# Kernel tuning notes

Measured on AMD Instinct MI355X. Metric: run time of the kernel, lower is better.

Reference implementation:

```python
import jax, jax.numpy as jnp
import numpy as np


def setup_inputs() -> dict:
    key = jax.random.key(0)
    k0, k1, k2 = jax.random.split(key, 3)
    B, C, N, M = 2, 64, 1024, 32
    C_mid = 16  # bottleneck of the AFA weight-learning MLP (C -> C//4 -> C)
    feature = jax.random.normal(k0, (B, C, N, M), dtype=jnp.float32)
    W1 = (jax.random.normal(k1, (C_mid, C), dtype=jnp.float32) / np.float32(np.sqrt(C)))
    b1 = jnp.zeros((C_mid,), dtype=jnp.float32)
    W2 = (jax.random.normal(k2, (C, C_mid), dtype=jnp.float32) / np.float32(np.sqrt(C_mid)))
    b2 = jnp.zeros((C,), dtype=jnp.float32)
    return {"feature": feature, "W1": W1, "b1": b1, "W2": W2, "b2": b2}


def reference(feature, W1, b1, W2, b2):
    # feature: (B, C, N, M)
    B, C, N, M = feature.shape
    eye = jnp.eye(M, dtype=feature.dtype)  # (M, M)
    # pair[b,c,n,i,j] = f_i - f_j + f_i * delta_ij  (the repeat/transpose/eye trick)
    fi = feature[..., :, None]                      # (B, C, N, M, 1)
    pair = fi - feature[..., None, :] + fi * eye    # (B, C, N, M, M)
    # 1x1-conv MLP over channel dim (SharedMLP: C -> C_mid -> C), ReLU between
    h = jax.nn.relu(jnp.einsum('oc,bcnij->bonij', W1, pair)
                    + b1[None, :, None, None, None])
    w = (jnp.einsum('oc,bcnij->bonij', W2, h)
         + b2[None, :, None, None, None])           # (B, C, N, M, M)
    w = jax.nn.softmax(w, axis=-1)                  # use_softmax=True, over last dim
    # weighted-sum aggregation over j -> (B, C, N, M)
    return jnp.sum(pair * w, axis=-1)
```

## Files before the change

### kernel.cpp

```cpp
#include <hip/hip_runtime.h>
#include <stdint.h>

namespace {
constexpr int NM = 1024 * 32;
constexpr float LOG2E = 1.44269504088896340736f;

typedef _Float16 half8 __attribute__((ext_vector_type(8)));
typedef float floatx16 __attribute__((ext_vector_type(16)));
typedef float f2v __attribute__((ext_vector_type(2)));

__device__ __forceinline__ uint32_t pkrtz_bits(float a, float b) {
  auto pk = __builtin_amdgcn_cvt_pkrtz(a, b);
  uint32_t u;
  __builtin_memcpy(&u, &pk, 4);
  return u;
}

__global__ __launch_bounds__(256, 4) void afa_kernel(
    const float* __restrict__ feat,
    const float* __restrict__ W1,
    const float* __restrict__ b1,
    const float* __restrict__ W2,
    float* __restrict__ out)
{
  __shared__ __align__(16) float f_c[64 * 34];
  __shared__ __align__(16) float g1b[32 * 20];
  __shared__ __align__(16) float edia[64 * 34];
  __shared__ __align__(16) float outs[64 * 34];

  const int t = threadIdx.x;
  const int bn = blockIdx.x;
  const size_t base = (size_t)(bn >> 10) * (64 * NM) + (size_t)(bn & 1023) * 32;

  const int w  = t >> 6;
  const int ln = t & 63;
  const int cl = ln & 31;
  const int hl = ln >> 5;

  half8 B0, B1;
  {
    const float4* w2a = reinterpret_cast<const float4*>(W2 + cl * 16 + 8 * hl);
    const float4 x = w2a[0], y = w2a[1];
    B0[0] = (_Float16)(x.x * LOG2E); B0[1] = (_Float16)(x.y * LOG2E);
    B0[2] = (_Float16)(x.z * LOG2E); B0[3] = (_Float16)(x.w * LOG2E);
    B0[4] = (_Float16)(y.x * LOG2E); B0[5] = (_Float16)(y.y * LOG2E);
    B0[6] = (_Float16)(y.z * LOG2E); B0[7] = (_Float16)(y.w * LOG2E);
    const float4* w2b = reinterpret_cast<const float4*>(W2 + (cl + 32) * 16 + 8 * hl);
    const float4 u = w2b[0], v = w2b[1];
    B1[0] = (_Float16)(u.x * LOG2E); B1[1] = (_Float16)(u.y * LOG2E);
    B1[2] = (_Float16)(u.z * LOG2E); B1[3] = (_Float16)(u.w * LOG2E);
    B1[4] = (_Float16)(v.x * LOG2E); B1[5] = (_Float16)(v.y * LOG2E);
    B1[6] = (_Float16)(v.z * LOG2E); B1[7] = (_Float16)(v.w * LOG2E);
  }

  {
    const int m = t & 31, c0 = t >> 5;
    #pragma unroll
    for (int r = 0; r < 8; ++r) {
      const int c = c0 + 8 * r;
      f_c[c * 34 + m] = feat[base + (size_t)c * NM + m];
    }
  }
  __syncthreads();

  floatx16 Z;
  #pragma unroll
  for (int r = 0; r < 16; ++r) Z[r] = 0.f;

  if (w == 0) {
    floatx16 Cg = Z;
    #pragma unroll
    for (int ch = 0; ch < 4; ++ch) {
      union { half8 h; uint32_t u[4]; } Af;
      if (cl < 16) {
        const float4 a0 = *reinterpret_cast<const float4*>(W1 + cl * 64 + 16 * ch + 8 * hl);
        const float4 a1 = *reinterpret_cast<const float4*>(W1 + cl * 64 + 16 * ch + 8 * hl + 4);
        Af.u[0] = pkrtz_bits(a0.x, a0.y);
        Af.u[1] = pkrtz_bits(a0.z, a0.w);
        Af.u[2] = pkrtz_bits(a1.x, a1.y);
        Af.u[3] = pkrtz_bits(a1.z, a1.w);
      } else {
        Af.u[0] = 0; Af.u[1] = 0; Af.u[2] = 0; Af.u[3] = 0;
      }
      union { half8 h; uint32_t u[4]; } Bf;
      #pragma unroll
      for (int p = 0; p < 4; ++p) {
        const int c = 16 * ch + 8 * hl + 2 * p;
        Bf.u[p] = pkrtz_bits(f_c[c * 34 + cl], f_c[(c + 1) * 34 + cl]);
      }
      Cg = __builtin_amdgcn_mfma_f32_32x32x16_f16(Af.h, Bf.h, Cg, 0, 0, 0);
    }
    const float4 bb0 = *reinterpret_cast<const float4*>(b1 + 4 * hl);
    const float4 bb1 = *reinterpret_cast<const float4*>(b1 + 8 + 4 * hl);
    const float4 g0 = {Cg[0] + bb0.x, Cg[1] + bb0.y, Cg[2] + bb0.z, Cg[3] + bb0.w};
    const float4 g1v = {Cg[4] + bb1.x, Cg[5] + bb1.y, Cg[6] + bb1.z, Cg[7] + bb1.w};
    *reinterpret_cast<float4*>(g1b + cl * 20 + 4 * hl) = g0;
    *reinterpret_cast<float4*>(g1b + cl * 20 + 8 + 4 * hl) = g1v;

    const uint32_t pk0 = pkrtz_bits(fmaxf(g0.x, 0.f), fmaxf(g0.y, 0.f));
    const uint32_t pk1 = pkrtz_bits(fmaxf(g0.z, 0.f), fmaxf(g0.w, 0.f));
    const uint32_t pk2 = pkrtz_bits(fmaxf(g1v.x, 0.f), fmaxf(g1v.y, 0.f));
    const uint32_t pk3 = pkrtz_bits(fmaxf(g1v.z, 0.f), fmaxf(g1v.w, 0.f));
    const uint32_t px0 = (uint32_t)__shfl_xor((int)pk0, 32);
    const uint32_t px1 = (uint32_t)__shfl_xor((int)pk1, 32);
    const uint32_t px2 = (uint32_t)__shfl_xor((int)pk2, 32);
    const uint32_t px3 = (uint32_t)__shfl_xor((int)pk3, 32);
    union { half8 h; uint32_t u[4]; } au;
    if (hl == 0) { au.u[0] = pk0; au.u[1] = pk1; au.u[2] = px0; au.u[3] = px1; }
    else         { au.u[0] = px2; au.u[1] = px3; au.u[2] = pk2; au.u[3] = pk3; }
    floatx16 d0 = __builtin_amdgcn_mfma_f32_32x32x16_f16(au.h, B0, Z, 0, 0, 0);
    floatx16 d1 = __builtin_amdgcn_mfma_f32_32x32x16_f16(au.h, B1, Z, 0, 0, 0);
    #pragma unroll
    for (int r = 0; r < 16; ++r) {
      const int ir = (r & 3) + 8 * (r >> 2) + 4 * hl;
      edia[cl * 34 + ir]        = __builtin_amdgcn_exp2f(d0[r]);
      edia[(cl + 32) * 34 + ir] = __builtin_amdgcn_exp2f(d1[r]);
    }
  }

  float fcol0[16], fcol1[16];
  #pragma unroll
  for (int q = 0; q < 4; ++q) {
    const int jr = 8 * q + 4 * hl;
    const float2 a0 = *reinterpret_cast<const float2*>(f_c + cl * 34 + jr);
    const float2 a1 = *reinterpret_cast<const float2*>(f_c + cl * 34 + jr + 2);
    fcol0[4 * q]     = a0.x; fcol0[4 * q + 1] = a0.y;
    fcol0[4 * q + 2] = a1.x; fcol0[4 * q + 3] = a1.y;
    const float2 c0v = *reinterpret_cast<const float2*>(f_c + (cl + 32) * 34 + jr);
    const float2 c1v = *reinterpret_cast<const float2*>(f_c + (cl + 32) * 34 + jr + 2);
    fcol1[4 * q]     = c0v.x; fcol1[4 * q + 1] = c0v.y;
    fcol1[4 * q + 2] = c1v.x; fcol1[4 * q + 3] = c1v.y;
  }
  __syncthreads();

  float gjn[8];
  {
    const float4* gp = reinterpret_cast<const float4*>(g1b + cl * 20 + 8 * hl);
    const float4 x = gp[0], y = gp[1];
    const float4* bb = reinterpret_cast<const float4*>(b1 + 8 * hl);
    const float4 bx = bb[0], by = bb[1];
    gjn[0] = bx.x - x.x; gjn[1] = bx.y - x.y; gjn[2] = bx.z - x.z; gjn[3] = bx.w - x.w;
    gjn[4] = by.x - y.x; gjn[5] = by.y - y.y; gjn[6] = by.z - y.z; gjn[7] = by.w - y.w;
  }

  #pragma unroll 1
  for (int ii = 0; ii < 8; ++ii) {
    const int i = w * 8 + ii;
    const bool dg = (cl == i);
    const float4* gi4 = reinterpret_cast<const float4*>(g1b + i * 20 + 8 * hl);
    const float4 gx = gi4[0], gy = gi4[1];
    const float gi[8] = {gx.x, gx.y, gx.z, gx.w, gy.x, gy.y, gy.z, gy.w};
    union { half8 h; uint32_t u[4]; } au;
    #pragma unroll
    for (int p = 0; p < 4; ++p) {
      const float h0 = fmaxf(gi[2 * p]     + (dg ? 0.f : gjn[2 * p]),     0.f);
      const float h1 = fmaxf(gi[2 * p + 1] + (dg ? 0.f : gjn[2 * p + 1]), 0.f);
      au.u[p] = pkrtz_bits(h0, h1);
    }
    const floatx16 acc0 = __builtin_amdgcn_mfma_f32_32x32x16_f16(au.h, B0, Z, 0, 0, 0);
    const floatx16 acc1 = __builtin_amdgcn_mfma_f32_32x32x16_f16(au.h, B1, Z, 0, 0, 0);

    f2v S0 = {0.f, 0.f}, D0 = {0.f, 0.f}, S1 = {0.f, 0.f}, D1 = {0.f, 0.f};
    #pragma unroll
    for (int r = 0; r < 16; r += 2) {
      const f2v e0 = {__builtin_amdgcn_exp2f(acc0[r]),
                      __builtin_amdgcn_exp2f(acc0[r + 1])};
      const f2v fc0 = {fcol0[r], fcol0[r + 1]};
      S0 += e0;
      D0 += fc0 * e0;
      const f2v e1 = {__builtin_amdgcn_exp2f(acc1[r]),
                      __builtin_amdgcn_exp2f(acc1[r + 1])};
      const f2v fc1 = {fcol1[r], fcol1[r + 1]};
      S1 += e1;
      D1 += fc1 * e1;
    }
    float Sa = S0.x + S0.y, Da = D0.x + D0.y;
    float Sb = S1.x + S1.y, Db = D1.x + D1.y;
    Sa += __shfl_xor(Sa, 32); Da += __shfl_xor(Da, 32);
    Sb += __shfl_xor(Sb, 32); Db += __shfl_xor(Db, 32);

    const float fi0 = f_c[cl * 34 + i];
    const float fi1 = f_c[(cl + 32) * 34 + i];
    const float ei0 = edia[cl * 34 + i];
    const float ei1 = edia[(cl + 32) * 34 + i];
    const float inv0 = 1.0f / Sa;
    const float inv1 = 1.0f / Sb;
    outs[cl * 34 + i]        = fi0 * (1.0f + ei0 * inv0) - Da * inv0;
    outs[(cl + 32) * 34 + i] = fi1 * (1.0f + ei1 * inv1) - Db * inv1;
  }
  __syncthreads();

  {
    const int m = t & 31, c0 = t >> 5;
    #pragma unroll
    for (int r = 0; r < 8; ++r) {
      const int cc = c0 + 8 * r;
      out[base + (size_t)cc * NM + m] = outs[cc * 34 + m];
    }
  }
}
}

extern "C" void kernel_launch(void* const* d_in, const int* in_sizes, int n_in,
                              void* d_out, int out_size, void* d_ws, size_t ws_size,
                              hipStream_t stream) {
  const float* feat = (const float*)d_in[0];
  const float* W1   = (const float*)d_in[1];
  const float* b1   = (const float*)d_in[2];
  const float* W2   = (const float*)d_in[3];
  float* out = (float*)d_out;

  afa_kernel<<<dim3(2 * 1024), dim3(256), 0, stream>>>(feat, W1, b1, W2, out);
}
```

Before: 31.21 us.

## Process both batches per block and prefetch second batch during first compute

Each block now handles one n index for both batch elements, which halves the grid. The second batch's features are loaded into registers before the first compute, so that global latency is hidden behind it. W2 fragment setup is also amortized over two tiles. In exchange, register pressure rises and there are fewer blocks for occupancy and tail balance.

```diff
diff --git a/kernel.cpp b/kernel.cpp
--- a/kernel.cpp
+++ b/kernel.cpp
@@ -29,13 +29,16 @@
   __shared__ __align__(16) float outs[64 * 34];
 
   const int t = threadIdx.x;
-  const int bn = blockIdx.x;
-  const size_t base = (size_t)(bn >> 10) * (64 * NM) + (size_t)(bn & 1023) * 32;
+  const int n = blockIdx.x;
+  const size_t base0 = (size_t)n * 32;
+  const size_t base1 = (size_t)64 * NM + (size_t)n * 32;
 
   const int w  = t >> 6;
   const int ln = t & 63;
   const int cl = ln & 31;
   const int hl = ln >> 5;
+  const int m  = t & 31;
+  const int c0 = t >> 5;
 
   half8 B0, B1;
   {
@@ -52,151 +55,167 @@
     B1[4] = (_Float16)(v.x * LOG2E); B1[5] = (_Float16)(v.y * LOG2E);
     B1[6] = (_Float16)(v.z * LOG2E); B1[7] = (_Float16)(v.w * LOG2E);
   }
-
-  {
-    const int m = t & 31, c0 = t >> 5;
+  floatx16 Z;
+  #pragma unroll
+  for (int r = 0; r < 16; ++r) Z[r] = 0.f;
+
+  #pragma unroll
+  for (int r = 0; r < 8; ++r) {
+    const int c = c0 + 8 * r;
+    f_c[c * 34 + m] = feat[base0 + (size_t)c * NM + m];
+  }
+  __syncthreads();
+
+  float p1s[8];
+  #pragma unroll
+  for (int r = 0; r < 8; ++r) {
+    const int c = c0 + 8 * r;
+    p1s[r] = feat[base1 + (size_t)c * NM + m];
+  }
+
+  auto compute = [&]() {
+    if (w == 0) {
+      floatx16 Cg = Z;
+      #pragma unroll
+      for (int ch = 0; ch < 4; ++ch) {
+        union { half8 h; uint32_t u[4]; } Af;
+        if (cl < 16) {
+          const float4 a0 = *reinterpret_cast<const float4*>(W1 + cl * 64 + 16 * ch + 8 * hl);
+          const float4 a1 = *reinterpret_cast<const float4*>(W1 + cl * 64 + 16 * ch + 8 * hl + 4);
+          Af.u[0] = pkrtz_bits(a0.x, a0.y);
+          Af.u[1] = pkrtz_bits(a0.z, a0.w);
+          Af.u[2] = pkrtz_bits(a1.x, a1.y);
+          Af.u[3] = pkrtz_bits(a1.z, a1.w);
+        } else {
+          Af.u[0] = 0; Af.u[1] = 0; Af.u[2] = 0; Af.u[3] = 0;
+        }
+        union { half8 h; uint32_t u[4]; } Bf;
+        #pragma unroll
+        for (int p = 0; p < 4; ++p) {
+          const int c = 16 * ch + 8 * hl + 2 * p;
+          Bf.u[p] = pkrtz_bits(f_c[c * 34 + cl], f_c[(c + 1) * 34 + cl]);
+        }
+        Cg = __builtin_amdgcn_mfma_f32_32x32x16_f16(Af.h, Bf.h, Cg, 0, 0, 0);
+      }
+      const float4 bb0 = *reinterpret_cast<const float4*>(b1 + 4 * hl);
+      const float4 bb1 = *reinterpret_cast<const float4*>(b1 + 8 + 4 * hl);
+      const float4 g0 = {Cg[0] + bb0.x, Cg[1] + bb0.y, Cg[2] + bb0.z, Cg[3] + bb0.w};
+      const float4 g1v = {Cg[4] + bb1.x, Cg[5] + bb1.y, Cg[6] + bb1.z, Cg[7] + bb1.w};
+      *reinterpret_cast<float4*>(g1b + cl * 20 + 4 * hl) = g0;
+      *reinterpret_cast<float4*>(g1b + cl * 20 + 8 + 4 * hl) = g1v;
+
+      const uint32_t pk0 = pkrtz_bits(fmaxf(g0.x, 0.f), fmaxf(g0.y, 0.f));
+      const uint32_t pk1 = pkrtz_bits(fmaxf(g0.z, 0.f), fmaxf(g0.w, 0.f));
+      const uint32_t pk2 = pkrtz_bits(fmaxf(g1v.x, 0.f), fmaxf(g1v.y, 0.f));
+      const uint32_t pk3 = pkrtz_bits(fmaxf(g1v.z, 0.f), fmaxf(g1v.w, 0.f));
+      const uint32_t px0 = (uint32_t)__shfl_xor((int)pk0, 32);
+      const uint32_t px1 = (uint32_t)__shfl_xor((int)pk1, 32);
+      const uint32_t px2 = (uint32_t)__shfl_xor((int)pk2, 32);
+      const uint32_t px3 = (uint32_t)__shfl_xor((int)pk3, 32);
+      union { half8 h; uint32_t u[4]; } au;
+      if (hl == 0) { au.u[0] = pk0; au.u[1] = pk1; au.u[2] = px0; au.u[3] = px1; }
+      else         { au.u[0] = px2; au.u[1] = px3; au.u[2] = pk2; au.u[3] = pk3; }
+      floatx16 d0 = __builtin_amdgcn_mfma_f32_32x32x16_f16(au.h, B0, Z, 0, 0, 0);
+      floatx16 d1 = __builtin_amdgcn_mfma_f32_32x32x16_f16(au.h, B1, Z, 0, 0, 0);
+      #pragma unroll
+      for (int r = 0; r < 16; ++r) {
+        const int ir = (r & 3) + 8 * (r >> 2) + 4 * hl;
+        edia[cl * 34 + ir]        = __builtin_amdgcn_exp2f(d0[r]);
+        edia[(cl + 32) * 34 + ir] = __builtin_amdgcn_exp2f(d1[r]);
+      }
+    }
+
+    float fcol0[16], fcol1[16];
     #pragma unroll
-    for (int r = 0; r < 8; ++r) {
-      const int c = c0 + 8 * r;
-      f_c[c * 34 + m] = feat[base + (size_t)c * NM + m];
-    }
+    for (int q = 0; q < 4; ++q) {
+      const int jr = 8 * q + 4 * hl;
+      const float2 a0 = *reinterpret_cast<const float2*>(f_c + cl * 34 + jr);
+      const float2 a1 = *reinterpret_cast<const float2*>(f_c + cl * 34 + jr + 2);
+      fcol0[4 * q]     = a0.x; fcol0[4 * q + 1] = a0.y;
+      fcol0[4 * q + 2] = a1.x; fcol0[4 * q + 3] = a1.y;
+      const float2 c0v = *reinterpret_cast<const float2*>(f_c + (cl + 32) * 34 + jr);
+      const float2 c1v = *reinterpret_cast<const float2*>(f_c + (cl + 32) * 34 + jr + 2);
+      fcol1[4 * q]     = c0v.x; fcol1[4 * q + 1] = c0v.y;
+      fcol1[4 * q + 2] = c1v.x; fcol1[4 * q + 3] = c1v.y;
+    }
+    __syncthreads();
+
+    float gjn[8];
+    {
+      const float4* gp = reinterpret_cast<const float4*>(g1b + cl * 20 + 8 * hl);
+      const float4 x = gp[0], y = gp[1];
+      const float4* bb = reinterpret_cast<const float4*>(b1 + 8 * hl);
+      const float4 bx = bb[0], by = bb[1];
+      gjn[0] = bx.x - x.x; gjn[1] = bx.y - x.y; gjn[2] = bx.z - x.z; gjn[3] = bx.w - x.w;
+      gjn[4] = by.x - y.x; gjn[5] = by.y - y.y; gjn[6] = by.z - y.z; gjn[7] = by.w - y.w;
+    }
+
+    #pragma unroll 1
+    for (int ii = 0; ii < 8; ++ii) {
+      const int i = w * 8 + ii;
+      const bool dg = (cl == i);
+      const float4* gi4 = reinterpret_cast<const float4*>(g1b + i * 20 + 8 * hl);
+      const float4 gx = gi4[0], gy = gi4[1];
+      const float gi[8] = {gx.x, gx.y, gx.z, gx.w, gy.x, gy.y, gy.z, gy.w};
+      union { half8 h; uint32_t u[4]; } au;
+      #pragma unroll
+      for (int p = 0; p < 4; ++p) {
+        const float h0 = fmaxf(gi[2 * p]     + (dg ? 0.f : gjn[2 * p]),     0.f);
+        const float h1 = fmaxf(gi[2 * p + 1] + (dg ? 0.f : gjn[2 * p + 1]), 0.f);
+        au.u[p] = pkrtz_bits(h0, h1);
+      }
+      const floatx16 acc0 = __builtin_amdgcn_mfma_f32_32x32x16_f16(au.h, B0, Z, 0, 0, 0);
+      const floatx16 acc1 = __builtin_amdgcn_mfma_f32_32x32x16_f16(au.h, B1, Z, 0, 0, 0);
+
+      f2v S0 = {0.f, 0.f}, D0 = {0.f, 0.f}, S1 = {0.f, 0.f}, D1 = {0.f, 0.f};
+      #pragma unroll
+      for (int r = 0; r < 16; r += 2) {
+        const f2v e0 = {__builtin_amdgcn_exp2f(acc0[r]),
+                        __builtin_amdgcn_exp2f(acc0[r + 1])};
+        const f2v fc0 = {fcol0[r], fcol0[r + 1]};
+        S0 += e0;
+        D0 += fc0 * e0;
+        const f2v e1 = {__builtin_amdgcn_exp2f(acc1[r]),
+                        __builtin_amdgcn_exp2f(acc1[r + 1])};
+        const f2v fc1 = {fcol1[r], fcol1[r + 1]};
+        S1 += e1;
+        D1 += fc1 * e1;
+      }
+      float Sa = S0.x + S0.y, Da = D0.x + D0.y;
+      float Sb = S1.x + S1.y, Db = D1.x + D1.y;
+      Sa += __shfl_xor(Sa, 32); Da += __shfl_xor(Da, 32);
+      Sb += __shfl_xor(Sb, 32); Db += __shfl_xor(Db, 32);
+
+      const float fi0 = f_c[cl * 34 + i];
+      const float fi1 = f_c[(cl + 32) * 34 + i];
+      const float ei0 = edia[cl * 34 + i];
+      const float ei1 = edia[(cl + 32) * 34 + i];
+      const float inv0 = 1.0f / Sa;
+      const float inv1 = 1.0f / Sb;
+      outs[cl * 34 + i]        = fi0 * (1.0f + ei0 * inv0) - Da * inv0;
+      outs[(cl + 32) * 34 + i] = fi1 * (1.0f + ei1 * inv1) - Db * inv1;
+    }
+    __syncthreads();
+  };
+
+  compute();
+  #pragma unroll
+  for (int r = 0; r < 8; ++r) {
+    const int c = c0 + 8 * r;
+    f_c[c * 34 + m] = p1s[r];
+  }
+  #pragma unroll
+  for (int r = 0; r < 8; ++r) {
+    const int cc = c0 + 8 * r;
+    out[base0 + (size_t)cc * NM + m] = outs[cc * 34 + m];
   }
   __syncthreads();
 
-  floatx16 Z;
-  #pragma unroll
-  for (int r = 0; r < 16; ++r) Z[r] = 0.f;
-
-  if (w == 0) {
-    floatx16 Cg = Z;
-    #pragma unroll
-    for (int ch = 0; ch < 4; ++ch) {
-      union { half8 h; uint32_t u[4]; } Af;
-      if (cl < 16) {
-        const float4 a0 = *reinterpret_cast<const float4*>(W1 + cl * 64 + 16 * ch + 8 * hl);
-        const float4 a1 = *reinterpret_cast<const float4*>(W1 + cl * 64 + 16 * ch + 8 * hl + 4);
-        Af.u[0] = pkrtz_bits(a0.x, a0.y);
-        Af.u[1] = pkrtz_bits(a0.z, a0.w);
-        Af.u[2] = pkrtz_bits(a1.x, a1.y);
-        Af.u[3] = pkrtz_bits(a1.z, a1.w);
-      } else {
-        Af.u[0] = 0; Af.u[1] = 0; Af.u[2] = 0; Af.u[3] = 0;
-      }
-      union { half8 h; uint32_t u[4]; } Bf;
-      #pragma unroll
-      for (int p = 0; p < 4; ++p) {
-        const int c = 16 * ch + 8 * hl + 2 * p;
-        Bf.u[p] = pkrtz_bits(f_c[c * 34 + cl], f_c[(c + 1) * 34 + cl]);
-      }
-      Cg = __builtin_amdgcn_mfma_f32_32x32x16_f16(Af.h, Bf.h, Cg, 0, 0, 0);
-    }
-    const float4 bb0 = *reinterpret_cast<const float4*>(b1 + 4 * hl);
-    const float4 bb1 = *reinterpret_cast<const float4*>(b1 + 8 + 4 * hl);
-    const float4 g0 = {Cg[0] + bb0.x, Cg[1] + bb0.y, Cg[2] + bb0.z, Cg[3] + bb0.w};
-    const float4 g1v = {Cg[4] + bb1.x, Cg[5] + bb1.y, Cg[6] + bb1.z, Cg[7] + bb1.w};
-    *reinterpret_cast<float4*>(g1b + cl * 20 + 4 * hl) = g0;
-    *reinterpret_cast<float4*>(g1b + cl * 20 + 8 + 4 * hl) = g1v;
-
-    const uint32_t pk0 = pkrtz_bits(fmaxf(g0.x, 0.f), fmaxf(g0.y, 0.f));
-    const uint32_t pk1 = pkrtz_bits(fmaxf(g0.z, 0.f), fmaxf(g0.w, 0.f));
-    const uint32_t pk2 = pkrtz_bits(fmaxf(g1v.x, 0.f), fmaxf(g1v.y, 0.f));
-    const uint32_t pk3 = pkrtz_bits(fmaxf(g1v.z, 0.f), fmaxf(g1v.w, 0.f));
-    const uint32_t px0 = (uint32_t)__shfl_xor((int)pk0, 32);
-    const uint32_t px1 = (uint32_t)__shfl_xor((int)pk1, 32);
-    const uint32_t px2 = (uint32_t)__shfl_xor((int)pk2, 32);
-    const uint32_t px3 = (uint32_t)__shfl_xor((int)pk3, 32);
-    union { half8 h; uint32_t u[4]; } au;
-    if (hl == 0) { au.u[0] = pk0; au.u[1] = pk1; au.u[2] = px0; au.u[3] = px1; }
-    else         { au.u[0] = px2; au.u[1] = px3; au.u[2] = pk2; au.u[3] = pk3; }
-    floatx16 d0 = __builtin_amdgcn_mfma_f32_32x32x16_f16(au.h, B0, Z, 0, 0, 0);
-    floatx16 d1 = __builtin_amdgcn_mfma_f32_32x32x16_f16(au.h, B1, Z, 0, 0, 0);
-    #pragma unroll
-    for (int r = 0; r < 16; ++r) {
-      const int ir = (r & 3) + 8 * (r >> 2) + 4 * hl;
-      edia[cl * 34 + ir]        = __builtin_amdgcn_exp2f(d0[r]);
-      edia[(cl + 32) * 34 + ir] = __builtin_amdgcn_exp2f(d1[r]);
-    }
-  }
-
-  float fcol0[16], fcol1[16];
-  #pragma unroll
-  for (int q = 0; q < 4; ++q) {
-    const int jr = 8 * q + 4 * hl;
-    const float2 a0 = *reinterpret_cast<const float2*>(f_c + cl * 34 + jr);
-    const float2 a1 = *reinterpret_cast<const float2*>(f_c + cl * 34 + jr + 2);
-    fcol0[4 * q]     = a0.x; fcol0[4 * q + 1] = a0.y;
-    fcol0[4 * q + 2] = a1.x; fcol0[4 * q + 3] = a1.y;
-    const float2 c0v = *reinterpret_cast<const float2*>(f_c + (cl + 32) * 34 + jr);
-    const float2 c1v = *reinterpret_cast<const float2*>(f_c + (cl + 32) * 34 + jr + 2);
-    fcol1[4 * q]     = c0v.x; fcol1[4 * q + 1] = c0v.y;
-    fcol1[4 * q + 2] = c1v.x; fcol1[4 * q + 3] = c1v.y;
-  }
-  __syncthreads();
-
-  float gjn[8];
-  {
-    const float4* gp = reinterpret_cast<const float4*>(g1b + cl * 20 + 8 * hl);
-    const float4 x = gp[0], y = gp[1];
-    const float4* bb = reinterpret_cast<const float4*>(b1 + 8 * hl);
-    const float4 bx = bb[0], by = bb[1];
-    gjn[0] = bx.x - x.x; gjn[1] = bx.y - x.y; gjn[2] = bx.z - x.z; gjn[3] = bx.w - x.w;
-    gjn[4] = by.x - y.x; gjn[5] = by.y - y.y; gjn[6] = by.z - y.z; gjn[7] = by.w - y.w;
-  }
-
-  #pragma unroll 1
-  for (int ii = 0; ii < 8; ++ii) {
-    const int i = w * 8 + ii;
-    const bool dg = (cl == i);
-    const float4* gi4 = reinterpret_cast<const float4*>(g1b + i * 20 + 8 * hl);
-    const float4 gx = gi4[0], gy = gi4[1];
-    const float gi[8] = {gx.x, gx.y, gx.z, gx.w, gy.x, gy.y, gy.z, gy.w};
-    union { half8 h; uint32_t u[4]; } au;
-    #pragma unroll
-    for (int p = 0; p < 4; ++p) {
-      const float h0 = fmaxf(gi[2 * p]     + (dg ? 0.f : gjn[2 * p]),     0.f);
-      const float h1 = fmaxf(gi[2 * p + 1] + (dg ? 0.f : gjn[2 * p + 1]), 0.f);
-      au.u[p] = pkrtz_bits(h0, h1);
-    }
-    const floatx16 acc0 = __builtin_amdgcn_mfma_f32_32x32x16_f16(au.h, B0, Z, 0, 0, 0);
-    const floatx16 acc1 = __builtin_amdgcn_mfma_f32_32x32x16_f16(au.h, B1, Z, 0, 0, 0);
-
-    f2v S0 = {0.f, 0.f}, D0 = {0.f, 0.f}, S1 = {0.f, 0.f}, D1 = {0.f, 0.f};
-    #pragma unroll
-    for (int r = 0; r < 16; r += 2) {
-      const f2v e0 = {__builtin_amdgcn_exp2f(acc0[r]),
-                      __builtin_amdgcn_exp2f(acc0[r + 1])};
-      const f2v fc0 = {fcol0[r], fcol0[r + 1]};
-      S0 += e0;
-      D0 += fc0 * e0;
-      const f2v e1 = {__builtin_amdgcn_exp2f(acc1[r]),
-                      __builtin_amdgcn_exp2f(acc1[r + 1])};
-      const f2v fc1 = {fcol1[r], fcol1[r + 1]};
-      S1 += e1;
-      D1 += fc1 * e1;
-    }
-    float Sa = S0.x + S0.y, Da = D0.x + D0.y;
-    float Sb = S1.x + S1.y, Db = D1.x + D1.y;
-    Sa += __shfl_xor(Sa, 32); Da += __shfl_xor(Da, 32);
-    Sb += __shfl_xor(Sb, 32); Db += __shfl_xor(Db, 32);
-
-    const float fi0 = f_c[cl * 34 + i];
-    const float fi1 = f_c[(cl + 32) * 34 + i];
-    const float ei0 = edia[cl * 34 + i];
-    const float ei1 = edia[(cl + 32) * 34 + i];
-    const float inv0 = 1.0f / Sa;
-    const float inv1 = 1.0f / Sb;
-    outs[cl * 34 + i]        = fi0 * (1.0f + ei0 * inv0) - Da * inv0;
-    outs[(cl + 32) * 34 + i] = fi1 * (1.0f + ei1 * inv1) - Db * inv1;
-  }
-  __syncthreads();
-
-  {
-    const int m = t & 31, c0 = t >> 5;
-    #pragma unroll
-    for (int r = 0; r < 8; ++r) {
-      const int cc = c0 + 8 * r;
-      out[base + (size_t)cc * NM + m] = outs[cc * 34 + m];
-    }
+  compute();
+  #pragma unroll
+  for (int r = 0; r < 8; ++r) {
+    const int cc = c0 + 8 * r;
+    out[base1 + (size_t)cc * NM + m] = outs[cc * 34 + m];
   }
 }
 }
@@ -210,5 +229,5 @@
   const float* W2   = (const float*)d_in[3];
   float* out = (float*)d_out;
 
-  afa_kernel<<<dim3(2 * 1024), dim3(256), 0, stream>>>(feat, W1, b1, W2, out);
-}
+  afa_kernel<<<dim3(1024), dim3(256), 0, stream>>>(feat, W1, b1, W2, out);
+}
```

New measurement: 33.05 us. 5.9% more time.
